# Kernel tuning notes

Measured on AMD Instinct MI355X. Metric: run time of the kernel, lower is better.

The kernel has to match this reference:

```python
import jax, jax.numpy as jnp
import numpy as np


def setup_inputs() -> dict:
    key = jax.random.key(0)
    k1, k2 = jax.random.split(key)
    N, K, D = 32768, 8192, 256
    inputs = jax.random.normal(k1, (N, D), dtype=jnp.float32)
    embedding = jax.random.normal(k2, (K, D), dtype=jnp.float32)  # codebook buffer
    return {"inputs": inputs, "embedding": embedding}


def reference(inputs, embedding):
    # distances[n, k] = ||x_n||^2 + ||e_k||^2 - 2 <x_n, e_k>   (squared L2, as in torch source)
    x_sq = jnp.sum(inputs * inputs, axis=1, keepdims=True)          # [N, 1]
    e_sq = jnp.sum(embedding * embedding, axis=1)                   # [K]
    cross = inputs @ embedding.T                                    # [N, K]
    distances = x_sq + e_sq - 2.0 * cross                           # [N, K]
    encoding_indices = jnp.argmin(distances, axis=1)                # [N] int
    # torch forward returns (None, None, indices); return the tensor output
    return encoding_indices
```

## Files before the change

kernel.cpp:

```cpp
#include <hip/hip_runtime.h>

constexpr int D_DIM   = 256;
constexpr int N_ROWS  = 32768;
constexpr int K_CODES = 8192;
constexpr unsigned TQ = 58;

typedef _Float16 f16x8  __attribute__((ext_vector_type(8)));
typedef __fp16   fp16x2 __attribute__((ext_vector_type(2)));
typedef float    f32x16 __attribute__((ext_vector_type(16)));

#define MFMA32(a, b, c) __builtin_amdgcn_mfma_f32_32x32x16_f16(a, b, c, 0, 0, 0)

__device__ __forceinline__ void cvt_rtn(const float4 a, const float4 b,
                                        uint4& hi, uint4& lo) {
    float f[8] = {a.x, a.y, a.z, a.w, b.x, b.y, b.z, b.w};
    unsigned hb[8], lb[8];
#pragma unroll
    for (int i = 0; i < 8; ++i) {
        _Float16 h = (_Float16)f[i];
        _Float16 l = (_Float16)(f[i] - (float)h);
        hb[i] = __builtin_bit_cast(unsigned short, h);
        lb[i] = __builtin_bit_cast(unsigned short, l);
    }
    hi = make_uint4(hb[0] | (hb[1] << 16), hb[2] | (hb[3] << 16),
                    hb[4] | (hb[5] << 16), hb[6] | (hb[7] << 16));
    lo = make_uint4(lb[0] | (lb[1] << 16), lb[2] | (lb[3] << 16),
                    lb[4] | (lb[5] << 16), lb[6] | (lb[7] << 16));
}

__device__ __forceinline__ void cvt_granule(const float4 a, const float4 b,
                                            uint4& hi, uint4& lo) {
    fp16x2 h0 = __builtin_amdgcn_cvt_pkrtz(a.x, a.y);
    fp16x2 h1 = __builtin_amdgcn_cvt_pkrtz(a.z, a.w);
    fp16x2 h2 = __builtin_amdgcn_cvt_pkrtz(b.x, b.y);
    fp16x2 h3 = __builtin_amdgcn_cvt_pkrtz(b.z, b.w);
    fp16x2 l0 = __builtin_amdgcn_cvt_pkrtz(a.x - (float)h0.x, a.y - (float)h0.y);
    fp16x2 l1 = __builtin_amdgcn_cvt_pkrtz(a.z - (float)h1.x, a.w - (float)h1.y);
    fp16x2 l2 = __builtin_amdgcn_cvt_pkrtz(b.x - (float)h2.x, b.y - (float)h2.y);
    fp16x2 l3 = __builtin_amdgcn_cvt_pkrtz(b.z - (float)h3.x, b.w - (float)h3.y);
    hi = make_uint4(__builtin_bit_cast(unsigned, h0), __builtin_bit_cast(unsigned, h1),
                    __builtin_bit_cast(unsigned, h2), __builtin_bit_cast(unsigned, h3));
    lo = make_uint4(__builtin_bit_cast(unsigned, l0), __builtin_bit_cast(unsigned, l1),
                    __builtin_bit_cast(unsigned, l2), __builtin_bit_cast(unsigned, l3));
}

__device__ __forceinline__ void gl_lds16(const uint4* g, uint4* l) {
    __builtin_amdgcn_global_load_lds(
        (const __attribute__((address_space(1))) void*)g,
        (__attribute__((address_space(3))) void*)l, 16, 0, 0);
}

__global__ __launch_bounds__(256)
void prep_kernel(const float* __restrict__ X, const float* __restrict__ E,
                 uint4* __restrict__ Xh,
                 uint4* __restrict__ Eh, uint4* __restrict__ El,
                 float* __restrict__ esqb, int* __restrict__ cnt) {
    const int tid = threadIdx.x, bid = blockIdx.x;
    if (bid < 1024) {
#pragma unroll 1
        for (int it = 0; it < 4; ++it) {
            const int gid = bid * 1024 + it * 256 + tid;
            const int rb = gid >> 11, rem = gid & 2047;
            const int Lg = rem >> 6, r = rem & 63;
            const float* p = X + (size_t)(rb * 64 + r) * D_DIM + Lg * 8;
            const float4 a = *(const float4*)p, b = *(const float4*)(p + 4);
            uint4 hi, lo; cvt_rtn(a, b, hi, lo);
            Xh[gid] = hi;
        }
    } else if (bid < 1280) {
#pragma unroll 1
        for (int it = 0; it < 4; ++it) {
            const int gid = (bid - 1024) * 1024 + it * 256 + tid;
            const int cb = gid >> 13, rem = gid & 8191;
            const int Lg = rem >> 8, c = rem & 255;
            const float* p = E + (size_t)(cb * 256 + c) * D_DIM + Lg * 8;
            const float4 a = *(const float4*)p, b = *(const float4*)(p + 4);
            uint4 hi, lo; cvt_rtn(a, b, hi, lo);
            Eh[gid] = hi; El[gid] = lo;
        }
    } else {
        if (bid == 1280 && tid == 0) *cnt = 0;
        const int t = (bid - 1280) * 256 + tid;
        const int gw = t >> 6, lane = t & 63;
        const float4 v = ((const float4*)(E + (size_t)gw * D_DIM))[lane];
        float s = v.x * v.x + v.y * v.y + v.z * v.z + v.w * v.w;
#pragma unroll
        for (int off = 32; off; off >>= 1) s += __shfl_down(s, off, 64);
        if (lane == 0) esqb[gw] = s + 1024.0f;
    }
}

__global__ __launch_bounds__(256, 2)
void vq_pass1(const uint4* __restrict__ Xh, const uint4* __restrict__ Eh,
              const float* __restrict__ esqb, uint2* __restrict__ res) {
    __shared__ uint4 sXh[2048];
    __shared__ uint2 slot[4][64];

    const int tid  = threadIdx.x;
    const int lane = tid & 63, wv = tid >> 6;
    const int l31  = lane & 31, lh = lane >> 5;
    const int bid  = blockIdx.x;
    const int bx = bid & 511, strip = bid >> 9;
    const int cs0 = strip * 2048;

    const uint4* Xhb = Xh + bx * 2048;

#pragma unroll
    for (int i = 0; i < 8; ++i)
        gl_lds16(Xhb + i * 256 + tid, &sXh[i * 256 + (wv << 6)]);
    __syncthreads();

    unsigned best[2][16], best2[2][16];
#pragma unroll
    for (int ti = 0; ti < 2; ++ti)
#pragma unroll
        for (int r = 0; r < 16; ++r) { best[ti][r] = 0xFFFFFFFFu; best2[ti][r] = 0xFFFFFFFFu; }

    f32x16 acc[2][2];

#pragma unroll 1
    for (int ct = 0; ct < 8; ++ct) {
        const uint4* __restrict__ Eb =
            Eh + (size_t)(strip * 8 + ct) * 8192 + wv * 64 + l31;

        const int code0 = cs0 + ct * 256 + wv * 64 + l31;
        const float eb0 = esqb[code0] * 128.0f;
        const float eb1 = esqb[code0 + 32] * 128.0f;

#pragma unroll
        for (int ti = 0; ti < 2; ++ti)
#pragma unroll
            for (int tj = 0; tj < 2; ++tj)
#pragma unroll
                for (int i = 0; i < 16; ++i) acc[ti][tj][i] = 0.0f;

#pragma unroll 1
        for (int h = 0; h < 2; ++h) {
            const int kb = h * 8;
            f16x8 b[16];
#pragma unroll
            for (int j = 0; j < 8; ++j) {
                const int Lg = (kb + j) * 2 + lh;
                b[j * 2]     = __builtin_bit_cast(f16x8, Eb[Lg * 256]);
                b[j * 2 + 1] = __builtin_bit_cast(f16x8, Eb[Lg * 256 + 32]);
            }
            __builtin_amdgcn_s_setprio(1);
#pragma unroll
            for (int k = 0; k < 8; ++k) {
                const int Lg = (kb + k) * 2 + lh;
                const f16x8 a0 = __builtin_bit_cast(f16x8, sXh[Lg * 64 + l31]);
                const f16x8 a1 = __builtin_bit_cast(f16x8, sXh[Lg * 64 + l31 + 32]);
                acc[0][0] = MFMA32(a0, b[k * 2],     acc[0][0]);
                acc[0][1] = MFMA32(a0, b[k * 2 + 1], acc[0][1]);
                acc[1][0] = MFMA32(a1, b[k * 2],     acc[1][0]);
                acc[1][1] = MFMA32(a1, b[k * 2 + 1], acc[1][1]);
            }
            __builtin_amdgcn_s_setprio(0);
        }

#pragma unroll
        for (int tj = 0; tj < 2; ++tj) {
            const unsigned code = (unsigned)(code0 + tj * 32);
            const float eb128 = tj ? eb1 : eb0;
#pragma unroll
            for (int ti = 0; ti < 2; ++ti)
#pragma unroll
                for (int r = 0; r < 16; ++r) {
                    const float dq = fmaf(-256.0f, acc[ti][tj][r], eb128);
                    const unsigned q   = (unsigned)dq;
                    const unsigned key = (q << 13) + code;
                    unsigned nb2;
                    asm("v_med3_u32 %0, %1, %2, %3"
                        : "=v"(nb2)
                        : "v"(key), "v"(best[ti][r]), "v"(best2[ti][r]));
                    best2[ti][r] = nb2;
                    best[ti][r]  = key < best[ti][r] ? key : best[ti][r];
                }
        }
    }

#pragma unroll
    for (int ti = 0; ti < 2; ++ti)
#pragma unroll
        for (int r = 0; r < 16; ++r) {
            unsigned b1 = best[ti][r], b2 = best2[ti][r];
#pragma unroll
            for (int m = 16; m >= 1; m >>= 1) {
                const unsigned o1 = (unsigned)__shfl_xor((int)b1, m, 32);
                const unsigned o2 = (unsigned)__shfl_xor((int)b2, m, 32);
                const unsigned t  = b1 > o1 ? b1 : o1;
                b1 = b1 < o1 ? b1 : o1;
                const unsigned m2 = b2 < o2 ? b2 : o2;
                b2 = m2 < t ? m2 : t;
            }
            if (l31 == 0) {
                const int row = ti * 32 + (r & 3) + 8 * (r >> 2) + 4 * lh;
                slot[wv][row] = make_uint2(b1, b2);
            }
        }

    __syncthreads();
    if (tid < 64) {
        const uint2 A = slot[0][tid];
        unsigned b1 = A.x, b2 = A.y;
#pragma unroll
        for (int s = 1; s < 4; ++s) {
            const uint2 B = slot[s][tid];
            const unsigned t  = b1 > B.x ? b1 : B.x;
            b1 = b1 < B.x ? b1 : B.x;
            const unsigned m2 = b2 < B.y ? b2 : B.y;
            b2 = m2 < t ? m2 : t;
        }
        res[(size_t)strip * N_ROWS + bx * 64 + tid] = make_uint2(b1, b2);
    }
}

__global__ void merge_kernel(const uint2* __restrict__ res,
                             unsigned long long* __restrict__ res0,
                             int* __restrict__ out,
                             int* __restrict__ cnt, int* __restrict__ list) {
    const int row = blockIdx.x * 256 + threadIdx.x;
    unsigned b1 = 0xFFFFFFFFu, b2 = 0xFFFFFFFFu;
#pragma unroll
    for (int s = 0; s < 4; ++s) {
        const uint2 v = res[(size_t)s * N_ROWS + row];
        const unsigned t = b1 > v.x ? b1 : v.x;
        b1 = b1 < v.x ? b1 : v.x;
        const unsigned m2 = b2 < v.y ? b2 : v.y;
        b2 = m2 < t ? m2 : t;
    }
    out[row] = (int)(b1 & 8191u);
    if ((b2 >> 13) - (b1 >> 13) < TQ) {
        const int p = atomicAdd(cnt, 1);
        list[p] = row;
        res0[row] = ~0ull;
    }
}

__global__ __launch_bounds__(256, 1)
void refine_kernel(const float* __restrict__ X,
                   const uint4* __restrict__ Eh, const uint4* __restrict__ El,
                   const float* __restrict__ esqb, const int* __restrict__ cnt,
                   const int* __restrict__ list, unsigned long long* __restrict__ res0) {
    __shared__ int  rows_s[32];
    __shared__ uint4 sAh[1024], sAl[1024];

    const int n = *cnt;
    const int base = blockIdx.x * 32;
    if (base >= n) return;
    const int tid = threadIdx.x;
    if (tid < 32) { const int j = base + tid; rows_s[tid] = list[j < n ? j : base]; }
    __syncthreads();

#pragma unroll
    for (int jj = 0; jj < 4; ++jj) {
        const int gg = jj * 256 + tid, Lg = gg >> 5, rr = gg & 31;
        const int row = rows_s[rr];
        const float* p = X + (size_t)row * D_DIM + Lg * 8;
        const float4 a = *(const float4*)p, b = *(const float4*)(p + 4);
        uint4 hi, lo; cvt_rtn(a, b, hi, lo);
        sAh[Lg * 32 + rr] = hi; sAl[Lg * 32 + rr] = lo;
    }
    __syncthreads();

    const int lane = tid & 63, wv = tid >> 6, l31 = lane & 31, lh = lane >> 5;
    const int cbase = blockIdx.y * 1024 + wv * 256;

    float bestv[16]; int besti[16];
#pragma unroll
    for (int r = 0; r < 16; ++r) { bestv[r] = 3.0e38f; besti[r] = 0; }

#pragma unroll 1
    for (int ps = 0; ps < 2; ++ps) {
        const int c0 = cbase + ps * 128;
        f32x16 acc[4];
#pragma unroll
        for (int tj = 0; tj < 4; ++tj)
#pragma unroll
            for (int i = 0; i < 16; ++i) acc[tj][i] = 0.0f;

#pragma unroll
        for (int ks = 0; ks < 16; ++ks) {
            const int Lg = ks * 2 + lh;
            f16x8 b0[4], b1[4];
#pragma unroll
            for (int tj = 0; tj < 4; ++tj) {
                const int c = c0 + tj * 32 + l31;
                const int eg = (c >> 8) * 8192 + Lg * 256 + (c & 255);
                b0[tj] = __builtin_bit_cast(f16x8, Eh[eg]);
                b1[tj] = __builtin_bit_cast(f16x8, El[eg]);
            }
            const f16x8 a0 = __builtin_bit_cast(f16x8, sAh[Lg * 32 + l31]);
            const f16x8 a1 = __builtin_bit_cast(f16x8, sAl[Lg * 32 + l31]);
#pragma unroll
            for (int tj = 0; tj < 4; ++tj) acc[tj] = MFMA32(a1, b0[tj], acc[tj]);
#pragma unroll
            for (int tj = 0; tj < 4; ++tj) acc[tj] = MFMA32(a0, b1[tj], acc[tj]);
#pragma unroll
            for (int tj = 0; tj < 4; ++tj) acc[tj] = MFMA32(a0, b0[tj], acc[tj]);
        }

#pragma unroll
        for (int tj = 0; tj < 4; ++tj) {
            const int c = c0 + tj * 32 + l31;
            const float eb = esqb[c];
#pragma unroll
            for (int r = 0; r < 16; ++r) {
                const float dv = fmaf(-2.0f, acc[tj][r], eb);
                if (dv < bestv[r]) { bestv[r] = dv; besti[r] = c; }
            }
        }
    }

#pragma unroll
    for (int r = 0; r < 16; ++r) {
        float v = bestv[r]; int bi = besti[r];
#pragma unroll
        for (int m = 16; m >= 1; m >>= 1) {
            const float ov = __shfl_xor(v, m, 32);
            const int   oi = __shfl_xor(bi, m, 32);
            if (ov < v || (ov == v && oi < bi)) { v = ov; bi = oi; }
        }
        if (l31 == 0) {
            const int rl = (r & 3) + 8 * (r >> 2) + 4 * lh;
            atomicMin(&res0[rows_s[rl]],
                      ((unsigned long long)__float_as_uint(v) << 32) | (unsigned)bi);
        }
    }
}

__global__ void finalize_kernel(const unsigned long long* __restrict__ res0,
                                const int* __restrict__ cnt, const int* __restrict__ list,
                                int* __restrict__ out) {
    const int i = blockIdx.x * 256 + threadIdx.x;
    if (i < *cnt) {
        const int row = list[i];
        out[row] = (int)(res0[row] & 0xFFFFFFFFull);
    }
}

__global__ void prologue_fb(const float* __restrict__ E, float* __restrict__ esqb,
                            unsigned long long* __restrict__ packed) {
    const int t = blockIdx.x * 256 + threadIdx.x;
    if (t < N_ROWS) packed[t] = ~0ull;
    const int gw = t >> 6, lane = t & 63;
    const float4 v = ((const float4*)(E + (size_t)gw * D_DIM))[lane];
    float s = v.x * v.x + v.y * v.y + v.z * v.z + v.w * v.w;
#pragma unroll
    for (int off = 32; off; off >>= 1) s += __shfl_down(s, off, 64);
    if (lane == 0) esqb[gw] = s + 1024.0f;
}

__global__ __launch_bounds__(256, 2)
void vq_mfma_fallback(const float* __restrict__ X, const float* __restrict__ E,
                      const float* __restrict__ esqb,
                      unsigned long long* __restrict__ packed) {
    __shared__ uint4 fXh[128 * 8], fXl[128 * 8];
    __shared__ uint4 fEh[128 * 8], fEl[128 * 8];
    __shared__ float fEsq[2048];

    const int tid  = threadIdx.x;
    const int lane = tid & 63;
    const int wv   = tid >> 6;
    const int wr   = wv >> 1, wc = wv & 1;
    const int l31  = lane & 31;
    const int lh   = lane >> 5;
    const int row0 = blockIdx.x * 128;
    const int cs0  = blockIdx.y * 2048;

#pragma unroll
    for (int i = 0; i < 8; ++i) fEsq[tid + 256 * i] = esqb[cs0 + tid + 256 * i];

    const int sr = tid >> 3, sg = tid & 7;

    float best[2][16]; int bidx[2][16];
#pragma unroll
    for (int ti = 0; ti < 2; ++ti)
#pragma unroll
        for (int r = 0; r < 16; ++r) { best[ti][r] = 3.0e38f; bidx[ti][r] = 0; }

    f32x16 acc[2][2];

#pragma unroll 1
    for (int ct = 0; ct < 16; ++ct) {
#pragma unroll
        for (int ti = 0; ti < 2; ++ti)
#pragma unroll
            for (int tj = 0; tj < 2; ++tj)
#pragma unroll
                for (int i = 0; i < 16; ++i) acc[ti][tj][i] = 0.0f;

#pragma unroll 1
        for (int dc = 0; dc < 4; ++dc) {
            __syncthreads();
#pragma unroll
            for (int i = 0; i < 4; ++i) {
                const int r = 32 * i + sr;
                const float* p = X + (size_t)(row0 + r) * D_DIM + dc * 64 + sg * 8;
                const float4 a = *(const float4*)p, b = *(const float4*)(p + 4);
                uint4 hi, lo; cvt_granule(a, b, hi, lo);
                const int o = r * 8 + (sg ^ (r & 7));
                fXh[o] = hi; fXl[o] = lo;
            }
#pragma unroll
            for (int i = 0; i < 4; ++i) {
                const int r = 32 * i + sr;
                const float* p = E + (size_t)(cs0 + ct * 128 + r) * D_DIM + dc * 64 + sg * 8;
                const float4 a = *(const float4*)p, b = *(const float4*)(p + 4);
                uint4 hi, lo; cvt_granule(a, b, hi, lo);
                const int o = r * 8 + (sg ^ (r & 7));
                fEh[o] = hi; fEl[o] = lo;
            }
            __syncthreads();

#pragma unroll
            for (int s = 0; s < 4; ++s) {
                const int gi = s * 2 + lh;
                f16x8 axh[2], axl[2], beh[2], bel[2];
#pragma unroll
                for (int ti = 0; ti < 2; ++ti) {
                    const int r = wr * 64 + ti * 32 + l31;
                    const int o = r * 8 + (gi ^ (r & 7));
                    axh[ti] = __builtin_bit_cast(f16x8, fXh[o]);
                    axl[ti] = __builtin_bit_cast(f16x8, fXl[o]);
                }
#pragma unroll
                for (int tj = 0; tj < 2; ++tj) {
                    const int c = wc * 64 + tj * 32 + l31;
                    const int o = c * 8 + (gi ^ (c & 7));
                    beh[tj] = __builtin_bit_cast(f16x8, fEh[o]);
                    bel[tj] = __builtin_bit_cast(f16x8, fEl[o]);
                }
#pragma unroll
                for (int ti = 0; ti < 2; ++ti)
#pragma unroll
                    for (int tj = 0; tj < 2; ++tj) {
                        acc[ti][tj] = MFMA32(axl[ti], beh[tj], acc[ti][tj]);
                        acc[ti][tj] = MFMA32(axh[ti], bel[tj], acc[ti][tj]);
                        acc[ti][tj] = MFMA32(axh[ti], beh[tj], acc[ti][tj]);
                    }
            }
        }

#pragma unroll
        for (int tj = 0; tj < 2; ++tj) {
            const int cloc = ct * 128 + wc * 64 + tj * 32 + l31;
            const float eb = fEsq[cloc];
            const int  code = cs0 + cloc;
#pragma unroll
            for (int ti = 0; ti < 2; ++ti)
#pragma unroll
                for (int r = 0; r < 16; ++r) {
                    const float dv = fmaf(-2.0f, acc[ti][tj][r], eb);
                    if (dv < best[ti][r]) { best[ti][r] = dv; bidx[ti][r] = code; }
                }
        }
    }

#pragma unroll
    for (int ti = 0; ti < 2; ++ti)
#pragma unroll
        for (int r = 0; r < 16; ++r) {
            float b = best[ti][r]; int bi = bidx[ti][r];
#pragma unroll
            for (int m = 16; m >= 1; m >>= 1) {
                const float ov = __shfl_xor(b, m, 32);
                const int   oi = __shfl_xor(bi, m, 32);
                if (ov < b || (ov == b && oi < bi)) { b = ov; bi = oi; }
            }
            if (l31 == 0) {
                const int row = row0 + wr * 64 + ti * 32 + (r & 3) + 8 * (r >> 2) + 4 * lh;
                const unsigned long long p =
                    ((unsigned long long)__float_as_uint(b) << 32) | (unsigned)bi;
                atomicMin(&packed[row], p);
            }
        }
}

__global__ void finish_fb(const unsigned long long* __restrict__ packed,
                          int* __restrict__ out) {
    const int i = blockIdx.x * 256 + threadIdx.x;
    out[i] = (int)(unsigned)(packed[i] & 0xffffffffull);
}

extern "C" void kernel_launch(void* const* d_in, const int* in_sizes, int n_in,
                              void* d_out, int out_size, void* d_ws, size_t ws_size,
                              hipStream_t stream) {
    const float* X = (const float*)d_in[0];
    const float* E = (const float*)d_in[1];
    char* ws = (char*)d_ws;
    int* out = (int*)d_out;

    float* esqb = (float*)ws;
    uint2* res  = (uint2*)(ws + 32768);
    unsigned long long* res0 = (unsigned long long*)(ws + 1081344);
    int* cnt  = (int*)(ws + 1343488);
    int* list = (int*)(ws + 1343504);
    const size_t base = 1572864;
    const size_t szX  = (size_t)N_ROWS * D_DIM * 2;
    const size_t szE  = (size_t)K_CODES * D_DIM * 2;
    const size_t need = base + szX + 2 * szE;

    if (ws_size >= need) {
        uint4* Xh = (uint4*)(ws + base);
        uint4* Eh = (uint4*)(ws + base + szX);
        uint4* El = (uint4*)(ws + base + szX + szE);
        prep_kernel<<<dim3(3328), dim3(256), 0, stream>>>(X, E, Xh, Eh, El, esqb, cnt);
        vq_pass1<<<dim3(2048), dim3(256), 0, stream>>>(Xh, Eh, esqb, res);
        merge_kernel<<<dim3(N_ROWS / 256), dim3(256), 0, stream>>>(res, res0, out, cnt, list);
        refine_kernel<<<dim3(1024, 8), dim3(256), 0, stream>>>(X, Eh, El, esqb,
                                                               cnt, list, res0);
        finalize_kernel<<<dim3(N_ROWS / 256), dim3(256), 0, stream>>>(res0, cnt, list, out);
    } else {
        unsigned long long* packed = (unsigned long long*)(ws + 32768);
        prologue_fb<<<dim3(2048), dim3(256), 0, stream>>>(E, esqb, packed);
        vq_mfma_fallback<<<dim3(N_ROWS / 128, 4), dim3(256), 0, stream>>>(X, E, esqb, packed);
        finish_fb<<<dim3(N_ROWS / 256), dim3(256), 0, stream>>>(packed, out);
    }
}
```

Baseline: 324.6 us.

## Retile pass1 block to 128 rows with 2x2 wave grid over codes

Each block now covers 128 input rows instead of 64, with the four waves arranged as 2 row groups by 2 code groups rather than 4 code groups. Every codebook tile loaded from global memory is therefore reused across twice as many rows, halving codebook traffic per row and halving the grid size. The cost is double the LDS for the X tile (64KB per block), which may limit occupancy below the two blocks per CU the launch bounds request, plus more code-tile iterations per block.

Result: faster. 308.0 us, median of 2 (-5.1%).

```diff
diff --git a/kernel.cpp b/kernel.cpp
--- a/kernel.cpp
+++ b/kernel.cpp
@@ -93,21 +93,21 @@
 __global__ __launch_bounds__(256, 2)
 void vq_pass1(const uint4* __restrict__ Xh, const uint4* __restrict__ Eh,
               const float* __restrict__ esqb, uint2* __restrict__ res) {
-    __shared__ uint4 sXh[2048];
-    __shared__ uint2 slot[4][64];
+    __shared__ uint4 sXh[4096];
+    __shared__ uint2 slot[2][128];
 
     const int tid  = threadIdx.x;
     const int lane = tid & 63, wv = tid >> 6;
+    const int wr = wv >> 1, wc = wv & 1;
     const int l31  = lane & 31, lh = lane >> 5;
     const int bid  = blockIdx.x;
-    const int bx = bid & 511, strip = bid >> 9;
+    const int bx = bid & 255, strip = bid >> 8;
     const int cs0 = strip * 2048;
 
-    const uint4* Xhb = Xh + bx * 2048;
-
-#pragma unroll
-    for (int i = 0; i < 8; ++i)
-        gl_lds16(Xhb + i * 256 + tid, &sXh[i * 256 + (wv << 6)]);
+#pragma unroll
+    for (int i = 0; i < 16; ++i)
+        gl_lds16(Xh + (size_t)(2 * bx + (wv & 1)) * 2048 + (2 * i + (wv >> 1)) * 64 + lane,
+                 &sXh[i * 256 + (wv << 6)]);
     __syncthreads();
 
     unsigned best[2][16], best2[2][16];
@@ -117,13 +117,14 @@
         for (int r = 0; r < 16; ++r) { best[ti][r] = 0xFFFFFFFFu; best2[ti][r] = 0xFFFFFFFFu; }
 
     f32x16 acc[2][2];
-
-#pragma unroll 1
-    for (int ct = 0; ct < 8; ++ct) {
+    const int arow = wr * 64 + l31;
+
+#pragma unroll 1
+    for (int ct = 0; ct < 16; ++ct) {
         const uint4* __restrict__ Eb =
-            Eh + (size_t)(strip * 8 + ct) * 8192 + wv * 64 + l31;
-
-        const int code0 = cs0 + ct * 256 + wv * 64 + l31;
+            Eh + (size_t)(strip * 8 + (ct >> 1)) * 8192 + (ct & 1) * 128 + wc * 64 + l31;
+
+        const int code0 = cs0 + ct * 128 + wc * 64 + l31;
         const float eb0 = esqb[code0] * 128.0f;
         const float eb1 = esqb[code0 + 32] * 128.0f;
 
@@ -148,8 +149,8 @@
 #pragma unroll
             for (int k = 0; k < 8; ++k) {
                 const int Lg = (kb + k) * 2 + lh;
-                const f16x8 a0 = __builtin_bit_cast(f16x8, sXh[Lg * 64 + l31]);
-                const f16x8 a1 = __builtin_bit_cast(f16x8, sXh[Lg * 64 + l31 + 32]);
+                const f16x8 a0 = __builtin_bit_cast(f16x8, sXh[Lg * 128 + arow]);
+                const f16x8 a1 = __builtin_bit_cast(f16x8, sXh[Lg * 128 + arow + 32]);
                 acc[0][0] = MFMA32(a0, b[k * 2],     acc[0][0]);
                 acc[0][1] = MFMA32(a0, b[k * 2 + 1], acc[0][1]);
                 acc[1][0] = MFMA32(a1, b[k * 2],     acc[1][0]);
@@ -194,24 +195,19 @@
                 b2 = m2 < t ? m2 : t;
             }
             if (l31 == 0) {
-                const int row = ti * 32 + (r & 3) + 8 * (r >> 2) + 4 * lh;
-                slot[wv][row] = make_uint2(b1, b2);
+                const int row = wr * 64 + ti * 32 + (r & 3) + 8 * (r >> 2) + 4 * lh;
+                slot[wc][row] = make_uint2(b1, b2);
             }
         }
 
     __syncthreads();
-    if (tid < 64) {
-        const uint2 A = slot[0][tid];
-        unsigned b1 = A.x, b2 = A.y;
-#pragma unroll
-        for (int s = 1; s < 4; ++s) {
-            const uint2 B = slot[s][tid];
-            const unsigned t  = b1 > B.x ? b1 : B.x;
-            b1 = b1 < B.x ? b1 : B.x;
-            const unsigned m2 = b2 < B.y ? b2 : B.y;
-            b2 = m2 < t ? m2 : t;
-        }
-        res[(size_t)strip * N_ROWS + bx * 64 + tid] = make_uint2(b1, b2);
+    if (tid < 128) {
+        const uint2 A = slot[0][tid], B = slot[1][tid];
+        const unsigned t  = A.x > B.x ? A.x : B.x;
+        const unsigned b1 = A.x < B.x ? A.x : B.x;
+        const unsigned m2 = A.y < B.y ? A.y : B.y;
+        const unsigned b2 = m2 < t ? m2 : t;
+        res[(size_t)strip * N_ROWS + bx * 128 + tid] = make_uint2(b1, b2);
     }
 }
 
@@ -506,7 +502,7 @@
         uint4* Eh = (uint4*)(ws + base + szX);
         uint4* El = (uint4*)(ws + base + szX + szE);
         prep_kernel<<<dim3(3328), dim3(256), 0, stream>>>(X, E, Xh, Eh, El, esqb, cnt);
-        vq_pass1<<<dim3(2048), dim3(256), 0, stream>>>(Xh, Eh, esqb, res);
+        vq_pass1<<<dim3(1024), dim3(256), 0, stream>>>(Xh, Eh, esqb, res);
         merge_kernel<<<dim3(N_ROWS / 256), dim3(256), 0, stream>>>(res, res0, out, cnt, list);
         refine_kernel<<<dim3(1024, 8), dim3(256), 0, stream>>>(X, Eh, El, esqb,
                                                                cnt, list, res0);
```
